# Optimization experiments

Hardware: AMD Instinct MI355X
Metric: run time of the kernel (lower is better)

Reference implementation:

```python
import jax, jax.numpy as jnp
import numpy as np

P = 2
SZ = 224
NIMG = 4
LX, LY, LF, LO = 32, 32, 3, 3
PL, PR, PT, PB = 16, 15, 16, 15
PFO = 1
NFREQ, NORIENT, NPHASE = 12, 8, 2
NFEAT = NPHASE * NORIENT * NFREQ  # 192
CX = SZ + PT + PB - LY + 1  # 224
CY = SZ + PL + PR - LX + 1  # 224


def _gauss(l, w):
    t = np.linspace(-1.0, 1.0, l)
    g = 1.0 / (np.sqrt(2.0 * np.pi) * w) * np.exp(-t ** 2 / (2.0 * w ** 2))
    return g.astype(np.float32)


def _conv2d(x, k):
    # x: [N,1,H,W], k: [1,1,kh,kw]; VALID cross-correlation, matching F.conv2d
    return jax.lax.conv_general_dilated(
        x, k, window_strides=(1, 1), padding='VALID',
        dimension_numbers=('NCHW', 'OIHW', 'NCHW'))


def setup_inputs() -> dict:
    key = jax.random.key(0)
    x = jax.random.normal(key, (NIMG, NFEAT, SZ, SZ), dtype=jnp.float32)
    return {"x": x}


def reference(x):
    gx = jnp.asarray(_gauss(LX, 1.0)).reshape(1, 1, 1, LX)
    gy = jnpy = jnp.asarray(_gauss(LY, 1.0)).reshape(1, 1, LY, 1)
    gf = jnp.asarray(_gauss(LF, 1.0)).reshape(1, 1, LF, 1)
    go = jnp.asarray(_gauss(LO, 1.0)).reshape(1, 1, 1, LO)

    x_p = x ** P
    x_p = jnp.pad(x_p, ((0, 0), (0, 0), (PT, PB), (PL, PR)))  # [B,192,255,255]
    # permute to [feat, img, H, W] then flatten features*imgs into batch
    t = jnp.transpose(x_p, (1, 0, 2, 3)).reshape(NFEAT * NIMG, 1, SZ + PT + PB, SZ + PL + PR)
    t = _conv2d(t, gx)  # [feat*img,1,255,224]
    t = _conv2d(t, gy)  # [feat*img,1,224,224]
    t = t.reshape(NFREQ, NORIENT, NPHASE, NIMG, 1, CX, CY)
    # -> [CX, CY, phase, img, 1, freq, orient]
    t = jnp.transpose(t, (5, 6, 2, 3, 4, 0, 1)).reshape(-1, 1, NFREQ, NORIENT)
    t = jnp.pad(t, ((0, 0), (0, 0), (PFO, PFO), (PFO, PFO)))  # [M,1,14,10]
    t = _conv2d(t, gf)  # [M,1,12,10]
    t = _conv2d(t, go)  # [M,1,12,8]
    B = t.reshape(CX, CY, NPHASE, NIMG, NFREQ, NORIENT)
    return jnp.transpose(B, (3, 4, 5, 2, 0, 1))  # [img,freq,orient,phase,CX,CY]
```

## Files before the change

kernel.cpp:

```cpp
#include <hip/hip_runtime.h>
#include <hip/hip_fp16.h>
#include <math.h>


#define SZW   224
#define PLANE (224*224)
#define PW    260

struct GaussArgs {
    float wx[32];
    float w30;
    float w31;
};

__device__ __forceinline__ int swz(int g) { return g ^ ((g >> 3) & 7); }

__global__ __launch_bounds__(512, 6) void pass1_kernel(const float* __restrict__ in,
                                                       __half* __restrict__ ws,
                                                       const GaussArgs ga)
{
    __shared__ float s2[48 * PW];

    const int tid   = threadIdx.x;
    const int y     = blockIdx.x;
    const int by    = blockIdx.y;
    const int phase = by & 1;
    const int fg    = by >> 1;
    const int img   = blockIdx.z;

    const float w31 = ga.w31;
    const float w30 = ga.w30;

    if (tid < 384) {
        const int lf  = tid >> 6;
        const int xp4 = tid & 63;
        const int f   = 4*fg - 1 + lf;
        const int gsw = swz(xp4);
        float4 a[8];
        if (f >= 0 && f < 12 && xp4 >= 4 && xp4 < 60) {
            const int x0 = xp4*4 - 16;
            const float* base = in + (size_t)(img*192 + f*16 + phase)*PLANE + y*SZW + x0;
            #pragma unroll
            for (int o = 0; o < 8; ++o) {
                float4 v = *reinterpret_cast<const float4*>(base + o*2*PLANE);
                a[o] = make_float4(v.x*v.x, v.y*v.y, v.z*v.z, v.w*v.w);
            }
        } else {
            #pragma unroll
            for (int o = 0; o < 8; ++o) a[o] = make_float4(0.f,0.f,0.f,0.f);
        }
        #pragma unroll
        for (int o = 0; o < 8; ++o) {
            float4 l = (o > 0) ? a[o-1] : make_float4(0.f,0.f,0.f,0.f);
            float4 r = (o < 7) ? a[o+1] : make_float4(0.f,0.f,0.f,0.f);
            float4 b;
            b.x = fmaf(w31, a[o].x, w30*(l.x + r.x));
            b.y = fmaf(w31, a[o].y, w30*(l.y + r.y));
            b.z = fmaf(w31, a[o].z, w30*(l.z + r.z));
            b.w = fmaf(w31, a[o].w, w30*(l.w + r.w));
            *reinterpret_cast<float4*>(&s2[(lf*8 + o)*PW + gsw*4]) = b;
        }
    }
    __syncthreads();

    {
        const int o   = tid >> 6;
        const int xp4 = tid & 63;
        const int gsw = swz(xp4);
        float4 a[6];
        #pragma unroll
        for (int lf = 0; lf < 6; ++lf)
            a[lf] = *reinterpret_cast<const float4*>(&s2[(lf*8 + o)*PW + gsw*4]);
        #pragma unroll
        for (int lf = 1; lf < 5; ++lf) {
            float4 b;
            b.x = fmaf(w31, a[lf].x, w30*(a[lf-1].x + a[lf+1].x));
            b.y = fmaf(w31, a[lf].y, w30*(a[lf-1].y + a[lf+1].y));
            b.z = fmaf(w31, a[lf].z, w30*(a[lf-1].z + a[lf+1].z));
            b.w = fmaf(w31, a[lf].w, w30*(a[lf-1].w + a[lf+1].w));
            *reinterpret_cast<float4*>(&s2[(lf*8 + o)*PW + gsw*4]) = b;
        }
    }
    __syncthreads();

    if (tid < 448) {
        const int r  = tid / 14;
        const int xg = tid - r*14;
        const int lf = 1 + (r >> 3);
        const int o  = r & 7;
        const int fo16 = (4*fg + (r >> 3))*16 + o*2;
        const int x0 = xg * 16;
        const int rowb = (lf*8 + o)*PW;
        const int g0 = 4*xg;

        float acc[16];
        #pragma unroll
        for (int j = 0; j < 16; ++j) acc[j] = 0.f;

        #pragma unroll
        for (int t = 0; t < 12; ++t) {
            const float4 q = *reinterpret_cast<const float4*>(
                &s2[rowb + swz(g0 + t)*4]);
            #pragma unroll
            for (int e = 0; e < 4; ++e) {
                const int m = 4*t + e;
                const float qv = (e==0)?q.x:(e==1)?q.y:(e==2)?q.z:q.w;
                const int jlo = (m - 31 > 0) ? (m - 31) : 0;
                const int jhi = (m < 15) ? m : 15;
                #pragma unroll
                for (int j = jlo; j <= jhi; ++j)
                    acc[j] = fmaf(ga.wx[m - j], qv, acc[j]);
            }
        }

        union { uint4 u4[2]; __half2 h2[8]; } pk;
        #pragma unroll
        for (int s = 0; s < 8; ++s)
            pk.h2[s] = __floats2half2_rn(acc[2*s], acc[2*s+1]);

        __half* op = ws + (size_t)(img*192 + phase)*PLANE + (size_t)y*SZW
                        + (size_t)fo16*PLANE + x0;
        *reinterpret_cast<uint4*>(op)     = pk.u4[0];
        *reinterpret_cast<uint4*>(op + 8) = pk.u4[1];
    }
}

__device__ __forceinline__ void p2_chunk(const __half* __restrict__ tile,
                                         const GaussArgs& ga,
                                         float* __restrict__ oc,
                                         int yb, int cc, int x0)
{
    const int sbase = cc * 14;
    float a0[14], a1[14];
    #pragma unroll
    for (int j = 0; j < 14; ++j) { a0[j] = 0.f; a1[j] = 0.f; }
    #pragma unroll
    for (int i = 0; i < 45; ++i) {
        const __half2 h = *reinterpret_cast<const __half2*>(&tile[(sbase + i)*SZW + x0]);
        const float2 f = __half22float2(h);
        const int jlo = (i - 31 > 0) ? (i - 31) : 0;
        const int jhi = (i < 13) ? i : 13;
        #pragma unroll
        for (int j = jlo; j <= jhi; ++j) {
            a0[j] = fmaf(ga.wx[i - j], f.x, a0[j]);
            a1[j] = fmaf(ga.wx[i - j], f.y, a1[j]);
        }
    }
    #pragma unroll
    for (int j = 0; j < 14; ++j)
        *reinterpret_cast<float2*>(oc + (size_t)(yb + cc*14 + j) * SZW) =
            make_float2(a0[j], a1[j]);
}

#define P2R 143
__global__ __launch_bounds__(512, 4) void pass2_kernel(const __half* __restrict__ ws,
                                                       float* __restrict__ out,
                                                       const GaussArgs ga)
{
    __shared__ __half tile[P2R * SZW];

    const int tid = threadIdx.x;
    const int ch  = blockIdx.x;
    const int yb  = blockIdx.y * 112;

    const __half* wp = ws + (size_t)ch * PLANE;

    for (int t = tid; t < P2R*28; t += 512) {
        const int r = t / 28;
        const int g = t - r*28;
        int yy = yb - 16 + r;
        yy = (yy < 0) ? 0 : (yy > SZW-1 ? SZW-1 : yy);
        __builtin_amdgcn_global_load_lds(
            (const __attribute__((address_space(1))) void*)(wp + (size_t)yy*SZW + g*8),
            (__attribute__((address_space(3))) void*)(&tile[(size_t)t*8]),
            16, 0, 0);
    }
    __syncthreads();

    if (blockIdx.y == 0) {
        for (int t = tid; t < 16*28; t += 512)
            *reinterpret_cast<uint4*>(&tile[(size_t)t*8]) = make_uint4(0u,0u,0u,0u);
    } else {
        for (int t = tid; t < 15*28; t += 512)
            *reinterpret_cast<uint4*>(&tile[(size_t)(128*28 + t)*8]) = make_uint4(0u,0u,0u,0u);
    }
    __syncthreads();

    if (tid < 448) {
        const int cp = tid % 112;
        const int gq = tid / 112;
        const int x0 = cp * 2;
        float* oc = out + (size_t)ch * PLANE + x0;

        p2_chunk(tile, ga, oc, yb, gq*2,     x0);
        p2_chunk(tile, ga, oc, yb, gq*2 + 1, x0);
    }
}

extern "C" void kernel_launch(void* const* d_in, const int* in_sizes, int n_in,
                              void* d_out, int out_size, void* d_ws, size_t ws_size,
                              hipStream_t stream)
{
    const float* x  = (const float*)d_in[0];
    float*      out = (float*)d_out;
    __half*     ws  = (__half*)d_ws;

    GaussArgs ga;
    const double c0 = 1.0 / sqrt(2.0 * 3.14159265358979323846);
    for (int k = 0; k < 32; ++k) {
        double t = -1.0 + 2.0 * (double)k / 31.0;
        ga.wx[k] = (float)(c0 * exp(-t * t / 2.0));
    }
    ga.w31 = (float)c0;
    ga.w30 = (float)(c0 * exp(-0.5));

    dim3 g1(SZW, 6, 4);
    pass1_kernel<<<g1, 512, 0, stream>>>(x, ws, ga);
    dim3 g2(768, 2);
    pass2_kernel<<<g2, 512, 0, stream>>>(ws, out, ga);
}
```

Baseline: 105.6 us.

## Stream pass2 tile loads through a zero row and overlap compute with loads

Pass1 now writes a zero row past the last plane in the workspace. Pass2 points its out-of-range halo loads at that row instead of clamping and zeroing afterwards, which removes the separate LDS zeroing step and one barrier. The tile load is split into eight unrolled async global-to-LDS copies. A partial vmcnt wait lets the first half of the row chunks compute while the later copies are still in flight. This relies on the ordering of the vmcnt counter, on the hand-placed waits matching the load order, and on the extra workspace row being available.

```diff
diff --git a/kernel.cpp b/kernel.cpp
--- a/kernel.cpp
+++ b/kernel.cpp
@@ -27,6 +27,10 @@
     const int phase = by & 1;
     const int fg    = by >> 1;
     const int img   = blockIdx.z;
+
+    if (blockIdx.x == 0 && by == 0 && img == 0 && tid < 28)
+        *reinterpret_cast<uint4*>(ws + (size_t)768 * PLANE + tid * 8) =
+            make_uint4(0u, 0u, 0u, 0u);
 
     const float w31 = ga.w31;
     const float w30 = ga.w30;
@@ -152,49 +156,54 @@
             make_float2(a0[j], a1[j]);
 }
 
-#define P2R 143
 __global__ __launch_bounds__(512, 4) void pass2_kernel(const __half* __restrict__ ws,
                                                        float* __restrict__ out,
                                                        const GaussArgs ga)
 {
-    __shared__ __half tile[P2R * SZW];
+    __shared__ __half tile[4096 * 8];
 
     const int tid = threadIdx.x;
     const int ch  = blockIdx.x;
     const int yb  = blockIdx.y * 112;
 
     const __half* wp = ws + (size_t)ch * PLANE;
-
-    for (int t = tid; t < P2R*28; t += 512) {
+    const __half* zr = ws + (size_t)768 * PLANE;
+
+    #pragma unroll
+    for (int k = 0; k < 8; ++k) {
+        const int t = tid + 512*k;
         const int r = t / 28;
         const int g = t - r*28;
-        int yy = yb - 16 + r;
-        yy = (yy < 0) ? 0 : (yy > SZW-1 ? SZW-1 : yy);
+        const int yy = yb - 16 + r;
+        const __half* src = (t < 4004 && yy >= 0 && yy < SZW)
+                          ? (wp + (size_t)yy*SZW + g*8)
+                          : (zr + g*8);
         __builtin_amdgcn_global_load_lds(
-            (const __attribute__((address_space(1))) void*)(wp + (size_t)yy*SZW + g*8),
+            (const __attribute__((address_space(1))) void*)src,
             (__attribute__((address_space(3))) void*)(&tile[(size_t)t*8]),
             16, 0, 0);
     }
-    __syncthreads();
-
-    if (blockIdx.y == 0) {
-        for (int t = tid; t < 16*28; t += 512)
-            *reinterpret_cast<uint4*>(&tile[(size_t)t*8]) = make_uint4(0u,0u,0u,0u);
-    } else {
-        for (int t = tid; t < 15*28; t += 512)
-            *reinterpret_cast<uint4*>(&tile[(size_t)(128*28 + t)*8]) = make_uint4(0u,0u,0u,0u);
-    }
-    __syncthreads();
-
-    if (tid < 448) {
-        const int cp = tid % 112;
-        const int gq = tid / 112;
-        const int x0 = cp * 2;
-        float* oc = out + (size_t)ch * PLANE + x0;
-
-        p2_chunk(tile, ga, oc, yb, gq*2,     x0);
-        p2_chunk(tile, ga, oc, yb, gq*2 + 1, x0);
-    }
+
+    asm volatile("s_waitcnt vmcnt(3)" ::: "memory");
+    __builtin_amdgcn_sched_barrier(0);
+    __builtin_amdgcn_s_barrier();
+    __builtin_amdgcn_sched_barrier(0);
+
+    const int cp = tid % 112;
+    const int gq = tid / 112;
+    const int x0 = cp * 2;
+    float* oc = out + (size_t)ch * PLANE + x0;
+
+    if (tid < 448)
+        p2_chunk(tile, ga, oc, yb, gq, x0);
+
+    asm volatile("s_waitcnt vmcnt(0)" ::: "memory");
+    __builtin_amdgcn_sched_barrier(0);
+    __builtin_amdgcn_s_barrier();
+    __builtin_amdgcn_sched_barrier(0);
+
+    if (tid < 448)
+        p2_chunk(tile, ga, oc, yb, 4 + gq, x0);
 }
 
 extern "C" void kernel_launch(void* const* d_in, const int* in_sizes, int n_in,
```

Result: no change. 107.6 us (+1.9%).
